# Performance work log

Measured on AMD Instinct MI355X. Metric: run time of the kernel, lower is better.

Reference implementation:

```python
import jax, jax.numpy as jnp
import numpy as np

# Mamba2 config fixed by the wrapper: state=32, expand=1, n_groups=1, conv kernel=4
H, P, N, K = 32, 64, 32, 4          # heads, head_dim, state_size, conv kernel
D_MODEL = H * P                      # hidden = intermediate (expand=1) = 2048
CONV_DIM = D_MODEL + 2 * N           # intermediate + 2*n_groups*state = 2112
PROJ = D_MODEL + CONV_DIM + H        # in_proj width = 4192
EPS = 1e-6


def setup_inputs() -> dict:
    key = jax.random.key(0)
    ks = jax.random.split(key, 8)
    B, L = 4, 2048
    w = lambda k, shape, sc=0.02: jax.random.normal(k, shape, jnp.float32) * sc
    return {
        "x": jax.random.normal(ks[0], (B, L, D_MODEL), jnp.float32),
        "W_in": w(ks[1], (D_MODEL, PROJ)),
        "b_in": jnp.zeros((PROJ,), jnp.float32),
        "conv_w": w(ks[2], (CONV_DIM, K), 0.25),
        "conv_b": jnp.zeros((CONV_DIM,), jnp.float32),
        "A_log": jnp.log(jnp.arange(1, H + 1, dtype=jnp.float32)),
        "dt_bias": jax.random.uniform(ks[3], (H,), jnp.float32, -4.0, 0.0),
        "D_param": jnp.ones((H,), jnp.float32),
        "norm_w": jnp.ones((D_MODEL,), jnp.float32),
        "W_out": w(ks[4], (D_MODEL, D_MODEL)),
    }


def reference(x, W_in, b_in, conv_w, conv_b, A_log, dt_bias, D_param, norm_w, W_out):
    B, L, _ = x.shape
    proj = x @ W_in + b_in                                   # (B,L,PROJ)
    gate, hBC, dt_raw = jnp.split(proj, [D_MODEL, D_MODEL + CONV_DIM], axis=-1)

    # causal depthwise conv1d over time (kernel K, left pad K-1), then SiLU
    hp = jnp.pad(hBC, ((0, 0), (K - 1, 0), (0, 0)))
    conv = conv_b + sum(hp[:, k:k + L, :] * conv_w[:, k] for k in range(K))
    conv = jax.nn.silu(conv)

    xs, Bm, Cm = jnp.split(conv, [D_MODEL, D_MODEL + N], axis=-1)
    xs = xs.reshape(B, L, H, P)                              # (B,L,H,P)

    A = -jnp.exp(A_log)                                      # (H,)
    dt = jax.nn.softplus(dt_raw + dt_bias)                   # (B,L,H)
    dA = jnp.exp(dt * A)                                     # (B,L,H)

    def step(hstate, inp):
        dA_t, dt_t, x_t, B_t, C_t = inp                      # (B,H),(B,H),(B,H,P),(B,N),(B,N)
        upd = (dt_t[:, :, None] * x_t)[..., None] * B_t[:, None, None, :]
        hstate = dA_t[:, :, None, None] * hstate + upd       # (B,H,P,N)
        y_t = jnp.einsum('bhpn,bn->bhp', hstate, C_t)
        return hstate, y_t

    h0 = jnp.zeros((B, H, P, N), x.dtype)
    scan_in = (dA.transpose(1, 0, 2), dt.transpose(1, 0, 2),
               xs.transpose(1, 0, 2, 3), Bm.transpose(1, 0, 2), Cm.transpose(1, 0, 2))
    _, ys = jax.lax.scan(step, h0, scan_in)                  # ys: (L,B,H,P)

    y = ys.transpose(1, 0, 2, 3) + D_param[None, None, :, None] * xs
    y = y.reshape(B, L, D_MODEL)

    # gated RMSNorm: gate applied before normalization (MambaRMSNormGated)
    y = y * jax.nn.silu(gate)
    var = jnp.mean(jnp.square(y), axis=-1, keepdims=True)
    y = y * jax.lax.rsqrt(var + EPS) * norm_w
    return y @ W_out
```

## Files before the change

### kernel.cpp

```cpp
#include <hip/hip_runtime.h>
#include <cstdint>
#include <cstddef>

constexpr int kB    = 4;
constexpr int kL    = 2048;
constexpr int kH    = 32;
constexpr int kP    = 64;
constexpr int kN    = 32;
constexpr int kD    = 2048;
constexpr int kProjW = 4192;
constexpr int kLdp  = 4224;
constexpr int kM    = kB * kL;
constexpr int kK    = kD;
constexpr int kLC   = 128;
constexpr int kNC   = kL / kLC;

typedef _Float16 f16x8 __attribute__((ext_vector_type(8)));
typedef float f32x4 __attribute__((ext_vector_type(4)));

__device__ __forceinline__ float lane_bcast(float v, int lane) {
    return __int_as_float(__builtin_amdgcn_readlane(__float_as_int(v), lane));
}
__device__ __forceinline__ float silu_f(float x) { return x / (1.f + __expf(-x)); }

__device__ __forceinline__ void async_copy16(const void* g, void* lds) {
    __builtin_amdgcn_global_load_lds(
        (const __attribute__((address_space(1))) unsigned int*)(uintptr_t)g,
        (__attribute__((address_space(3))) unsigned int*)(uintptr_t)lds,
        16, 0, 0);
}

__global__ __launch_bounds__(256) void cast_f16_kernel(const float* __restrict__ in,
                                                       _Float16* __restrict__ out) {
    size_t i = ((size_t)blockIdx.x * 256 + threadIdx.x) * 8;
    float4 a = *(const float4*)(in + i);
    float4 b = *(const float4*)(in + i + 4);
    f16x8 o;
    o[0] = (_Float16)a.x; o[1] = (_Float16)a.y; o[2] = (_Float16)a.z; o[3] = (_Float16)a.w;
    o[4] = (_Float16)b.x; o[5] = (_Float16)b.y; o[6] = (_Float16)b.z; o[7] = (_Float16)b.w;
    *(f16x8*)(out + i) = o;
}

__global__ __launch_bounds__(256) void transpose_cast_kernel(const float* __restrict__ W,
                                                             _Float16* __restrict__ Wt,
                                                             int R, int C) {
    __shared__ float tile[32][33];
    const int c0 = blockIdx.x * 32;
    const int r0 = blockIdx.y * 32;
    const int tx = threadIdx.x & 31;
    const int ty = threadIdx.x >> 5;
    #pragma unroll
    for (int i = 0; i < 32; i += 8) {
        int rr = r0 + ty + i;
        int cc = c0 + tx;
        tile[ty + i][tx] = (cc < C) ? W[(size_t)rr * C + cc] : 0.f;
    }
    __syncthreads();
    #pragma unroll
    for (int i = 0; i < 32; i += 8) {
        int cc = c0 + ty + i;
        int rr = r0 + tx;
        Wt[(size_t)cc * R + rr] = (_Float16)tile[tx][ty + i];
    }
}

template <bool OUT_F16>
__global__ __launch_bounds__(256, 2) void gemm_bt_kernel(
    const _Float16* __restrict__ A, const _Float16* __restrict__ Bt,
    const float* __restrict__ bias, int nbias,
    void* __restrict__ Cout, int K, int ldc, float* __restrict__ dtside)
{
    __shared__ __attribute__((aligned(16))) _Float16 As[3][256 * 32];
    __shared__ __attribute__((aligned(16))) _Float16 Bs[3][128 * 32];

    const int tid = threadIdx.x;
    const int w   = tid >> 6;
    const int l   = tid & 63;
    const int r   = l & 15;
    const int q   = l >> 4;

    const int pid = blockIdx.x;
    const int i0  = pid >> 3;
    const int m_idx = (pid & 7) * 4 + (i0 & 3);
    const int n_idx = i0 >> 2;

    const size_t tileM = (size_t)m_idx * 256;
    const size_t tileN = (size_t)n_idx * 128;

    const _Float16* gA[4];
    #pragma unroll
    for (int g = 0; g < 4; ++g)
        gA[g] = A + (tileM + (size_t)((w + g * 4) * 16 + r)) * K + q * 8;
    const _Float16* gB[2];
    #pragma unroll
    for (int g = 0; g < 2; ++g)
        gB[g] = Bt + (tileN + (size_t)((w + g * 4) * 16 + r)) * K + q * 8;

    auto stage = [&](int s, int koff) {
        #pragma unroll
        for (int g = 0; g < 4; ++g)
            async_copy16(gA[g] + koff, &As[s][(w + g * 4) * 512]);
        #pragma unroll
        for (int g = 0; g < 2; ++g)
            async_copy16(gB[g] + koff, &Bs[s][(w + g * 4) * 512]);
    };

    const int T = K >> 5;
    stage(0, 0);
    stage(1, 32);

    f32x4 acc[4][8] = {};
    int cs = 0;

    for (int k = 0; k < T; ++k) {
        if (k + 1 < T) asm volatile("s_waitcnt vmcnt(6)" ::: "memory");
        else           asm volatile("s_waitcnt vmcnt(0)" ::: "memory");
        asm volatile("s_barrier" ::: "memory");
        if (k + 2 < T) {
            int ns = cs + 2; if (ns >= 3) ns -= 3;
            stage(ns, (k + 2) * 32);
        }
        f16x8 af[4], bf[8];
        #pragma unroll
        for (int i = 0; i < 4; ++i)
            af[i] = *(const f16x8*)&As[cs][(w * 4 + i) * 512 + l * 8];
        #pragma unroll
        for (int j = 0; j < 8; ++j)
            bf[j] = *(const f16x8*)&Bs[cs][j * 512 + l * 8];
        #pragma unroll
        for (int i = 0; i < 4; ++i)
            #pragma unroll
            for (int j = 0; j < 8; ++j)
                acc[i][j] = __builtin_amdgcn_mfma_f32_16x16x32_f16(af[i], bf[j], acc[i][j], 0, 0, 0);
        cs = (cs + 1 >= 3) ? 0 : cs + 1;
    }

    #pragma unroll
    for (int j = 0; j < 8; ++j) {
        const int col = (int)tileN + j * 16 + r;
        float bv = 0.f;
        if (bias != nullptr && col < nbias) bv = bias[col];
        #pragma unroll
        for (int i = 0; i < 4; ++i) {
            const size_t row = tileM + (size_t)(w * 64 + i * 16 + q * 4);
            #pragma unroll
            for (int u = 0; u < 4; ++u) {
                float v = acc[i][j][u] + bv;
                if (OUT_F16) ((_Float16*)Cout)[(row + u) * ldc + col] = (_Float16)v;
                else         ((float*)Cout)[(row + u) * ldc + col] = v;
                if (dtside != nullptr && col >= 4160 && col < 4192)
                    dtside[(row + u) * 32 + (col - 4160)] = v;
            }
        }
    }
}

__global__ __launch_bounds__(256) void dt_da_kernel(
    const float* __restrict__ dtraw, const float* __restrict__ A_log,
    const float* __restrict__ dt_bias, float* __restrict__ dtv, float* __restrict__ dAv)
{
    int idx = blockIdx.x * 256 + threadIdx.x;
    int t  = idx & (kL - 1);
    int bh = idx >> 11;
    int h  = bh & (kH - 1);
    int b  = bh >> 5;
    float z  = dtraw[((size_t)(b * kL + t)) * kH + h] + dt_bias[h];
    float dt = (z > 20.f) ? z : log1pf(expf(z));
    float dA = expf(dt * -expf(A_log[h]));
    dtv[idx] = dt;
    dAv[idx] = dA;
}

__global__ __launch_bounds__(64) void scan_pass1_kernel(
    const _Float16* __restrict__ projh, const float* __restrict__ conv_w,
    const float* __restrict__ conv_b, const float* __restrict__ dtv,
    const float* __restrict__ dAv, float* __restrict__ cstate, float* __restrict__ Pch)
{
    const int blk = blockIdx.x;
    const int c   = blk & (kNC - 1);
    const int bh  = blk >> 4;
    const int h   = bh & (kH - 1);
    const int b   = bh >> 5;
    const int l   = threadIdx.x;
    const int t0  = c * kLC;

    const int chx = h * kP + l;
    const int chb = 2048 + (l & 31);
    const float xw0 = conv_w[chx*4+0], xw1 = conv_w[chx*4+1], xw2 = conv_w[chx*4+2], xw3 = conv_w[chx*4+3];
    const float xbb = conv_b[chx];
    const float bw0 = conv_w[chb*4+0], bw1 = conv_w[chb*4+1], bw2 = conv_w[chb*4+2], bw3 = conv_w[chb*4+3];
    const float bbb = conv_b[chb];

    const _Float16* pb = projh + (size_t)b * kL * kLdp;
    const int colx = 2048 + chx;
    const int colb = 2048 + chb;

    float xq0=0.f, xq1=0.f, xq2=0.f, bq0=0.f, bq1=0.f, bq2=0.f;
    if (c > 0) {
        xq0 = (float)pb[(size_t)(t0-3)*kLdp + colx];
        xq1 = (float)pb[(size_t)(t0-2)*kLdp + colx];
        xq2 = (float)pb[(size_t)(t0-1)*kLdp + colx];
        bq0 = (float)pb[(size_t)(t0-3)*kLdp + colb];
        bq1 = (float)pb[(size_t)(t0-2)*kLdp + colb];
        bq2 = (float)pb[(size_t)(t0-1)*kLdp + colb];
    }

    float hs[kN];
    #pragma unroll
    for (int n = 0; n < kN; ++n) hs[n] = 0.f;
    float Pp = 1.f;
    const float* dtp = dtv + (size_t)bh * kL;
    const float* dAp = dAv + (size_t)bh * kL;

    #pragma unroll 1
    for (int t = t0; t < t0 + kLC; ++t) {
        const size_t ro = (size_t)t * kLdp;
        float xv = (float)pb[ro + colx];
        float bv = (float)pb[ro + colb];
        float sx = silu_f(xbb + xw0*xq0 + xw1*xq1 + xw2*xq2 + xw3*xv);
        float sb = silu_f(bbb + bw0*bq0 + bw1*bq1 + bw2*bq2 + bw3*bv);
        xq0=xq1; xq1=xq2; xq2=xv;
        bq0=bq1; bq1=bq2; bq2=bv;
        float dt = dtp[t], dA = dAp[t];
        float dtx = dt * sx;
        Pp *= dA;
        #pragma unroll
        for (int n = 0; n < kN; ++n)
            hs[n] = fmaf(dA, hs[n], dtx * lane_bcast(sb, n));
    }
    float* cs = cstate + (size_t)blk * (kP * kN) + l * kN;
    #pragma unroll
    for (int n = 0; n < kN; ++n) cs[n] = hs[n];
    if (l == 0) Pch[blk] = Pp;
}

__global__ __launch_bounds__(256) void scan_pass2_kernel(float* __restrict__ cstate,
                                                         const float* __restrict__ Pch) {
    const int bh  = blockIdx.x;
    const int off = threadIdx.x * 8;
    float s[8];
    #pragma unroll
    for (int i = 0; i < 8; ++i) s[i] = 0.f;
    float* base = cstate + (size_t)bh * (kNC * kP * kN) + off;
    #pragma unroll 1
    for (int c = 0; c < kNC; ++c) {
        float* cs = base + c * (kP * kN);
        float Pp = Pch[bh * kNC + c];
        #pragma unroll
        for (int i = 0; i < 8; ++i) {
            float loc = cs[i];
            cs[i] = s[i];
            s[i] = fmaf(Pp, s[i], loc);
        }
    }
}

__global__ __launch_bounds__(64) void scan_pass3_kernel(
    const _Float16* __restrict__ projh, const float* __restrict__ conv_w,
    const float* __restrict__ conv_b, const float* __restrict__ dtv,
    const float* __restrict__ dAv, const float* __restrict__ cstate,
    const float* __restrict__ D_param, float* __restrict__ ypre)
{
    const int blk = blockIdx.x;
    const int c   = blk & (kNC - 1);
    const int bh  = blk >> 4;
    const int h   = bh & (kH - 1);
    const int b   = bh >> 5;
    const int l   = threadIdx.x;
    const int t0  = c * kLC;

    const int chx = h * kP + l;
    const int chc = 2048 + l;
    const float xw0 = conv_w[chx*4+0], xw1 = conv_w[chx*4+1], xw2 = conv_w[chx*4+2], xw3 = conv_w[chx*4+3];
    const float xbb = conv_b[chx];
    const float cw0 = conv_w[chc*4+0], cw1 = conv_w[chc*4+1], cw2 = conv_w[chc*4+2], cw3 = conv_w[chc*4+3];
    const float cbb = conv_b[chc];

    const _Float16* pb = projh + (size_t)b * kL * kLdp;
    const int colx = 2048 + chx;
    const int colc = 2048 + chc;

    float xq0=0.f, xq1=0.f, xq2=0.f, cq0=0.f, cq1=0.f, cq2=0.f;
    if (c > 0) {
        xq0 = (float)pb[(size_t)(t0-3)*kLdp + colx];
        xq1 = (float)pb[(size_t)(t0-2)*kLdp + colx];
        xq2 = (float)pb[(size_t)(t0-1)*kLdp + colx];
        cq0 = (float)pb[(size_t)(t0-3)*kLdp + colc];
        cq1 = (float)pb[(size_t)(t0-2)*kLdp + colc];
        cq2 = (float)pb[(size_t)(t0-1)*kLdp + colc];
    }

    float hs[kN];
    const float* cs = cstate + (size_t)blk * (kP * kN) + l * kN;
    #pragma unroll
    for (int n = 0; n < kN; ++n) hs[n] = cs[n];
    const float Dh = D_param[h];
    const float* dtp = dtv + (size_t)bh * kL;
    const float* dAp = dAv + (size_t)bh * kL;
    float* yo = ypre + (size_t)b * kL * kD + h * kP + l;

    #pragma unroll 1
    for (int t = t0; t < t0 + kLC; ++t) {
        const size_t ro = (size_t)t * kLdp;
        float xv = (float)pb[ro + colx];
        float cv = (float)pb[ro + colc];
        float sx = silu_f(xbb + xw0*xq0 + xw1*xq1 + xw2*xq2 + xw3*xv);
        float sc = silu_f(cbb + cw0*cq0 + cw1*cq1 + cw2*cq2 + cw3*cv);
        xq0=xq1; xq1=xq2; xq2=xv;
        cq0=cq1; cq1=cq2; cq2=cv;
        float dt = dtp[t], dA = dAp[t];
        float dtx = dt * sx;
        float y0 = Dh * sx, y1 = 0.f;
        #pragma unroll
        for (int n = 0; n < kN; ++n) {
            float bn = lane_bcast(sc, n);
            float cn = lane_bcast(sc, n + 32);
            hs[n] = fmaf(dA, hs[n], dtx * bn);
            if (n & 1) y1 = fmaf(hs[n], cn, y1);
            else       y0 = fmaf(hs[n], cn, y0);
        }
        yo[(size_t)t * kD] = y0 + y1;
    }
}

__global__ __launch_bounds__(256) void gated_norm_kernel(
    const float* __restrict__ ypre, const _Float16* __restrict__ projh,
    const float* __restrict__ norm_w, _Float16* __restrict__ yh)
{
    const int row = blockIdx.x;
    const int tid = threadIdx.x;
    const float* yr = ypre + (size_t)row * kD;
    const _Float16* gr = projh + (size_t)row * kLdp;
    float v[8];
    float ss = 0.f;
    #pragma unroll
    for (int u = 0; u < 8; ++u) {
        int col = tid + u * 256;
        float g = (float)gr[col];
        float t = yr[col] * (g / (1.f + __expf(-g)));
        v[u] = t;
        ss = fmaf(t, t, ss);
    }
    #pragma unroll
    for (int off = 32; off > 0; off >>= 1) ss += __shfl_xor(ss, off, 64);
    __shared__ float red[4];
    if ((tid & 63) == 0) red[tid >> 6] = ss;
    __syncthreads();
    float tot = (red[0] + red[1]) + (red[2] + red[3]);
    float scl = rsqrtf(tot * (1.f / (float)kD) + 1e-6f);
    #pragma unroll
    for (int u = 0; u < 8; ++u) {
        int col = tid + u * 256;
        yh[(size_t)row * kD + col] = (_Float16)(v[u] * scl * norm_w[col]);
    }
}

extern "C" void kernel_launch(void* const* d_in, const int* in_sizes, int n_in,
                              void* d_out, int out_size, void* d_ws, size_t ws_size,
                              hipStream_t stream)
{
    (void)in_sizes; (void)n_in; (void)out_size; (void)ws_size;
    const float* x       = (const float*)d_in[0];
    const float* W_in    = (const float*)d_in[1];
    const float* b_in    = (const float*)d_in[2];
    const float* conv_w  = (const float*)d_in[3];
    const float* conv_b  = (const float*)d_in[4];
    const float* A_log   = (const float*)d_in[5];
    const float* dt_bias = (const float*)d_in[6];
    const float* D_param = (const float*)d_in[7];
    const float* norm_w  = (const float*)d_in[8];
    const float* W_out   = (const float*)d_in[9];
    float* out = (float*)d_out;

    char* p = (char*)d_ws;
    _Float16* projh = (_Float16*)p; p += (size_t)kM * kLdp * 2;
    _Float16* xh    = (_Float16*)p; p += (size_t)kM * kD * 2;
    _Float16* Wt    = (_Float16*)p; p += (size_t)kLdp * kK * 2;
    _Float16* Wot   = (_Float16*)p; p += (size_t)kD * kK * 2;
    float* dtraw    = (float*)p;    p += (size_t)kM * kH * 4;
    float* dtv      = (float*)p;    p += (size_t)kB * kH * kL * 4;
    float* dAv      = (float*)p;    p += (size_t)kB * kH * kL * 4;
    float* cstate   = (float*)p;    p += (size_t)kB * kH * kNC * kP * kN * 4;
    float* Pch      = (float*)p;    p += (size_t)kB * kH * kNC * 4;
    _Float16* yh = xh;
    float* ypre = out;

    cast_f16_kernel<<<(kM * kD) / (256 * 8), 256, 0, stream>>>(x, xh);
    transpose_cast_kernel<<<dim3(kLdp / 32, kK / 32), 256, 0, stream>>>(W_in, Wt, kK, kProjW);
    transpose_cast_kernel<<<dim3(kD / 32, kK / 32), 256, 0, stream>>>(W_out, Wot, kK, kD);
    gemm_bt_kernel<true><<<(kM / 256) * (kLdp / 128), 256, 0, stream>>>(
        xh, Wt, b_in, kProjW, (void*)projh, kK, kLdp, dtraw);
    dt_da_kernel<<<(kB * kH * kL) / 256, 256, 0, stream>>>(dtraw, A_log, dt_bias, dtv, dAv);
    scan_pass1_kernel<<<kB * kH * kNC, 64, 0, stream>>>(projh, conv_w, conv_b, dtv, dAv, cstate, Pch);
    scan_pass2_kernel<<<kB * kH, 256, 0, stream>>>(cstate, Pch);
    scan_pass3_kernel<<<kB * kH * kNC, 64, 0, stream>>>(projh, conv_w, conv_b, dtv, dAv, cstate, D_param, ypre);
    gated_norm_kernel<<<kM, 256, 0, stream>>>(ypre, projh, norm_w, yh);
    gemm_bt_kernel<false><<<(kM / 256) * (kD / 128), 256, 0, stream>>>(
        yh, Wot, nullptr, 0, (void*)out, kK, kD, nullptr);
}
```

Baseline: 734.2 us.

## Double-buffer GEMM LDS fragments in registers to overlap LDS reads with MFMA

Restructures the fp16 MFMA GEMM main loop so the next k-step's A/B fragments are loaded from LDS into a second register set while the current step's MFMAs execute, unrolling by two with ping-pong register buffers. It also issues the next global->LDS stage before the wait. The aim is to hide LDS read latency behind matrix math. In exchange it doubles fragment register use, which may lower occupancy, and relies on T being even.

```diff
diff --git a/kernel.cpp b/kernel.cpp
--- a/kernel.cpp
+++ b/kernel.cpp
@@ -109,31 +109,53 @@
     stage(0, 0);
     stage(1, 32);
 
+    f16x8 fa0[4], fb0[8], fa1[4], fb1[8];
     f32x4 acc[4][8] = {};
+
+    asm volatile("s_waitcnt vmcnt(6)" ::: "memory");
+    asm volatile("s_barrier" ::: "memory");
+    #pragma unroll
+    for (int i = 0; i < 4; ++i) fa0[i] = *(const f16x8*)&As[0][(w * 4 + i) * 512 + l * 8];
+    #pragma unroll
+    for (int j = 0; j < 8; ++j) fb0[j] = *(const f16x8*)&Bs[0][j * 512 + l * 8];
+
     int cs = 0;
 
-    for (int k = 0; k < T; ++k) {
-        if (k + 1 < T) asm volatile("s_waitcnt vmcnt(6)" ::: "memory");
-        else           asm volatile("s_waitcnt vmcnt(0)" ::: "memory");
-        asm volatile("s_barrier" ::: "memory");
-        if (k + 2 < T) {
-            int ns = cs + 2; if (ns >= 3) ns -= 3;
-            stage(ns, (k + 2) * 32);
-        }
-        f16x8 af[4], bf[8];
-        #pragma unroll
-        for (int i = 0; i < 4; ++i)
-            af[i] = *(const f16x8*)&As[cs][(w * 4 + i) * 512 + l * 8];
-        #pragma unroll
-        for (int j = 0; j < 8; ++j)
-            bf[j] = *(const f16x8*)&Bs[cs][j * 512 + l * 8];
-        #pragma unroll
-        for (int i = 0; i < 4; ++i)
-            #pragma unroll
-            for (int j = 0; j < 8; ++j)
-                acc[i][j] = __builtin_amdgcn_mfma_f32_16x16x32_f16(af[i], bf[j], acc[i][j], 0, 0, 0);
-        cs = (cs + 1 >= 3) ? 0 : cs + 1;
-    }
+#define GEMM_BODY(KIDX, CA, CB, NA, NB)                                          \
+    {                                                                            \
+        const int k_ = (KIDX);                                                   \
+        if (k_ + 2 < T) {                                                        \
+            int ss = cs + 2; if (ss >= 3) ss -= 3;                               \
+            stage(ss, (k_ + 2) * 32);                                            \
+            asm volatile("s_waitcnt vmcnt(6)" ::: "memory");                     \
+        } else {                                                                 \
+            asm volatile("s_waitcnt vmcnt(0)" ::: "memory");                     \
+        }                                                                        \
+        asm volatile("s_waitcnt lgkmcnt(0)" ::: "memory");                       \
+        asm volatile("s_barrier" ::: "memory");                                  \
+        int nsl = cs + 1; if (nsl >= 3) nsl -= 3;                                \
+        if (k_ + 1 < T) {                                                        \
+            _Pragma("unroll")                                                    \
+            for (int i = 0; i < 4; ++i)                                          \
+                NA[i] = *(const f16x8*)&As[nsl][(w * 4 + i) * 512 + l * 8];      \
+            _Pragma("unroll")                                                    \
+            for (int j = 0; j < 8; ++j)                                          \
+                NB[j] = *(const f16x8*)&Bs[nsl][j * 512 + l * 8];                \
+        }                                                                        \
+        _Pragma("unroll")                                                        \
+        for (int i = 0; i < 4; ++i)                                              \
+            _Pragma("unroll")                                                    \
+            for (int j = 0; j < 8; ++j)                                          \
+                acc[i][j] = __builtin_amdgcn_mfma_f32_16x16x32_f16(              \
+                    CA[i], CB[j], acc[i][j], 0, 0, 0);                           \
+        cs = nsl;                                                                \
+    }
+
+    for (int k = 0; k < T; k += 2) {
+        GEMM_BODY(k,     fa0, fb0, fa1, fb1)
+        GEMM_BODY(k + 1, fa1, fb1, fa0, fb0)
+    }
+#undef GEMM_BODY
 
     #pragma unroll
     for (int j = 0; j < 8; ++j) {
```

New measurement: 736.1 us. About the same (+0.3%).
